# Kernel tuning notes

Hardware: AMD Instinct MI355X
Metric: run time of the kernel (lower is better)

The kernel has to match this reference:

```python
import jax, jax.numpy as jnp
import numpy as np

D_MODEL = 1024
NUM_HEADS = 16
HEAD_DIM = D_MODEL // NUM_HEADS
B, S = 2, 2048


def setup_inputs() -> dict:
    key = jax.random.key(0)
    ks = jax.random.split(key, 12)
    s = 0.02
    inp = {
        "Q": jax.random.normal(ks[0], (B, S, D_MODEL), jnp.float32),
        "K": jax.random.normal(ks[1], (B, S, D_MODEL), jnp.float32),
        "V": jax.random.normal(ks[2], (B, S, D_MODEL), jnp.float32),
        # causal mask: 1 = keep, 0 = masked (matches masked_fill(mask == 0, -inf))
        "mask": jnp.tril(jnp.ones((S, S), jnp.int32))[None, None, :, :],
        "Wq": jax.random.normal(ks[3], (D_MODEL, D_MODEL), jnp.float32) * s,
        "bq": jnp.zeros((D_MODEL,), jnp.float32),
        "Wk": jax.random.normal(ks[4], (D_MODEL, D_MODEL), jnp.float32) * s,
        "bk": jnp.zeros((D_MODEL,), jnp.float32),
        "Wv": jax.random.normal(ks[5], (D_MODEL, D_MODEL), jnp.float32) * s,
        "bv": jnp.zeros((D_MODEL,), jnp.float32),
        "Wo": jax.random.normal(ks[6], (D_MODEL, D_MODEL), jnp.float32) * s,
        "bo": jnp.zeros((D_MODEL,), jnp.float32),
    }
    return inp


def reference(Q, K, V, mask, Wq, bq, Wk, bk, Wv, bv, Wo, bo):
    b, sq, _ = Q.shape
    sk = K.shape[1]
    # linear projections (torch Linear: x @ W^T + b)
    q = Q @ Wq.T + bq
    k = K @ Wk.T + bk
    v = V @ Wv.T + bv
    # [B, H, S, Dh]
    q = q.reshape(b, sq, NUM_HEADS, HEAD_DIM).transpose(0, 2, 1, 3)
    k = k.reshape(b, sk, NUM_HEADS, HEAD_DIM).transpose(0, 2, 1, 3)
    v = v.reshape(b, sk, NUM_HEADS, HEAD_DIM).transpose(0, 2, 1, 3)
    scores = jnp.einsum("bhqd,bhkd->bhqk", q, k) / jnp.sqrt(
        jnp.asarray(HEAD_DIM, q.dtype)
    )
    scores = jnp.where(mask == 0, jnp.asarray(-jnp.inf, scores.dtype), scores)
    attn = jax.nn.softmax(scores, axis=-1)
    out = jnp.einsum("bhqk,bhkd->bhqd", attn, v)
    out = out.transpose(0, 2, 1, 3).reshape(b, sq, D_MODEL)
    return out @ Wo.T + bo
```

## Files before the change

kernel.cpp:

```cpp
#include <hip/hip_runtime.h>
#include <hip/hip_bf16.h>
#include <cstdint>
#include <cstddef>


typedef __attribute__((ext_vector_type(8))) short bf16x8;
typedef __attribute__((ext_vector_type(4))) short bf16x4;
typedef __attribute__((ext_vector_type(4))) float f32x4;
typedef __attribute__((ext_vector_type(2))) unsigned int u32x2;

constexpr int GM = 4096;
constexpr int GN = 1024;
constexpr int GK = 1024;
#define QSCALE 0.18033688011112042f

#if __has_builtin(__builtin_amdgcn_mfma_f32_16x16x16bf16_1k)
#define MFMA16(a, b, c) __builtin_amdgcn_mfma_f32_16x16x16bf16_1k((a), (b), (c), 0, 0, 0)
#elif __has_builtin(__builtin_amdgcn_mfma_f32_16x16x16_bf16)
#define MFMA16(a, b, c) __builtin_amdgcn_mfma_f32_16x16x16_bf16((a), (b), (c), 0, 0, 0)
#else
static __device__ __forceinline__ f32x4 mfma16_asm(bf16x4 a, bf16x4 b, f32x4 c) {
  asm volatile("v_mfma_f32_16x16x16_bf16 %0, %1, %2, %0" : "+v"(c) : "v"(a), "v"(b));
  return c;
}
#define MFMA16(a, b, c) mfma16_asm((a), (b), (c))
#endif

#if __has_builtin(__builtin_amdgcn_exp2f)
#define EXP2(x) __builtin_amdgcn_exp2f(x)
#else
#define EXP2(x) exp2f(x)
#endif

__device__ __forceinline__ void gload_lds16(const __hip_bfloat16* g, __hip_bfloat16* l) {
  __builtin_amdgcn_global_load_lds(
      (const __attribute__((address_space(1))) void*)g,
      (__attribute__((address_space(3))) void*)l, 16, 0, 0);
}

__device__ __forceinline__ unsigned lds_off(const void* p) {
  return (unsigned)(uintptr_t)(__attribute__((address_space(3))) const void*)p;
}

__global__ __launch_bounds__(256) void cvt7_kernel(
    const float* __restrict__ a0, const float* __restrict__ a1,
    const float* __restrict__ a2, const float* __restrict__ a3,
    const float* __restrict__ a4, const float* __restrict__ a5,
    const float* __restrict__ a6,
    __hip_bfloat16* __restrict__ o0, __hip_bfloat16* __restrict__ o1,
    __hip_bfloat16* __restrict__ o2, __hip_bfloat16* __restrict__ o3,
    __hip_bfloat16* __restrict__ o4, __hip_bfloat16* __restrict__ o5,
    __hip_bfloat16* __restrict__ o6) {
  const int z = blockIdx.z;
  const int n8 = (z < 3) ? 524288 : 131072;
  int i = blockIdx.x * 256 + threadIdx.x;
  if (i >= n8) return;
  const float* in;
  __hip_bfloat16* out;
  switch (z) {
    case 0: in = a0; out = o0; break;
    case 1: in = a1; out = o1; break;
    case 2: in = a2; out = o2; break;
    case 3: in = a3; out = o3; break;
    case 4: in = a4; out = o4; break;
    case 5: in = a5; out = o5; break;
    default: in = a6; out = o6; break;
  }
  const float4* p = (const float4*)in;
  float4 a = p[i * 2];
  float4 c = p[i * 2 + 1];
  union { __hip_bfloat16 h[8]; bf16x8 v; } u;
  u.h[0] = __float2bfloat16(a.x); u.h[1] = __float2bfloat16(a.y);
  u.h[2] = __float2bfloat16(a.z); u.h[3] = __float2bfloat16(a.w);
  u.h[4] = __float2bfloat16(c.x); u.h[5] = __float2bfloat16(c.y);
  u.h[6] = __float2bfloat16(c.z); u.h[7] = __float2bfloat16(c.w);
  *(bf16x8*)(out + (size_t)i * 8) = u.v;
}

__global__ __launch_bounds__(256) void qkv_gemm_kernel(
    const __hip_bfloat16* __restrict__ Xq, const __hip_bfloat16* __restrict__ Xk,
    const __hip_bfloat16* __restrict__ Xv,
    const __hip_bfloat16* __restrict__ Wq, const __hip_bfloat16* __restrict__ Wk,
    const __hip_bfloat16* __restrict__ Wv,
    const float* __restrict__ bq, const float* __restrict__ bk,
    const float* __restrict__ bv,
    __hip_bfloat16* __restrict__ oq, __hip_bfloat16* __restrict__ ok,
    __hip_bfloat16* __restrict__ ov) {
  __shared__ __align__(16) __hip_bfloat16 Asm[128 * 32];
  __shared__ __align__(16) __hip_bfloat16 Bsm[128 * 32];
  const int tid = threadIdx.x;
  const int l = tid & 63, w = tid >> 6;
  const int lo = l & 15, hi = l >> 4;
  const int wr = w >> 1, wc = w & 1;
  const int widx = blockIdx.x >> 3;
  const int n0 = (blockIdx.x & 7) * 128;
  const int m0 = blockIdx.y * 128;
  const int srow = (l >> 2), scol = (l & 3) * 8;

  const __hip_bfloat16* A  = (widx == 0) ? Xq : (widx == 1) ? Xk : Xv;
  const __hip_bfloat16* Bw = (widx == 0) ? Wq : (widx == 1) ? Wk : Wv;
  const float* bias        = (widx == 0) ? bq : (widx == 1) ? bk : bv;
  __hip_bfloat16* C        = (widx == 0) ? oq : (widx == 1) ? ok : ov;
  const float oscale       = (widx == 0) ? QSCALE : 1.0f;

  f32x4 acc[4][4] = {};

  for (int kt = 0; kt < GK; kt += 32) {
#pragma unroll
    for (int i = 0; i < 2; ++i) {
      const int c = i * 4 + w;
      const int row = c * 16 + srow;
      gload_lds16(A + (size_t)(m0 + row) * GK + kt + scol, &Asm[c * 512]);
      gload_lds16(Bw + (size_t)(n0 + row) * GK + kt + scol, &Bsm[c * 512]);
    }
    __syncthreads();
    bf16x8 af[4], bfr[4];
#pragma unroll
    for (int f = 0; f < 4; ++f) {
      af[f]  = *(const bf16x8*)&Asm[(wr * 64 + f * 16 + lo) * 32 + hi * 8];
      bfr[f] = *(const bf16x8*)&Bsm[(wc * 64 + f * 16 + lo) * 32 + hi * 8];
    }
#pragma unroll
    for (int i = 0; i < 4; ++i)
#pragma unroll
      for (int j = 0; j < 4; ++j)
        acc[i][j] = __builtin_amdgcn_mfma_f32_16x16x32_bf16(af[i], bfr[j], acc[i][j], 0, 0, 0);
    __syncthreads();
  }

#pragma unroll
  for (int i = 0; i < 4; ++i) {
#pragma unroll
    for (int j = 0; j < 4; ++j) {
      const int gc = n0 + wc * 64 + j * 16 + lo;
      const float bs = bias[gc];
#pragma unroll
      for (int r = 0; r < 4; ++r) {
        const int gr = m0 + wr * 64 + i * 16 + hi * 4 + r;
        C[(size_t)gr * GN + gc] = __float2bfloat16((acc[i][j][r] + bs) * oscale);
      }
    }
  }
}

__global__ __launch_bounds__(256) void gemm_out_kernel(
    const __hip_bfloat16* __restrict__ A,
    const __hip_bfloat16* __restrict__ Bw,
    const float* __restrict__ bias, float* __restrict__ C) {
  __shared__ __align__(16) __hip_bfloat16 Asm[64 * 32];
  __shared__ __align__(16) __hip_bfloat16 Bsm[128 * 32];
  const int tid = threadIdx.x;
  const int l = tid & 63, w = tid >> 6;
  const int lo = l & 15, hi = l >> 4;
  const int wr = w >> 1, wc = w & 1;
  const int m0 = blockIdx.y * 64, n0 = blockIdx.x * 128;
  const int srowA = (l >> 2), scol = (l & 3) * 8;

  f32x4 acc[2][4] = {};

  for (int kt = 0; kt < GK; kt += 32) {
    {
      const int rowA = w * 16 + srowA;
      gload_lds16(A + (size_t)(m0 + rowA) * GK + kt + scol, &Asm[w * 512]);
    }
#pragma unroll
    for (int i = 0; i < 2; ++i) {
      const int c = i * 4 + w;
      const int row = c * 16 + srowA;
      gload_lds16(Bw + (size_t)(n0 + row) * GK + kt + scol, &Bsm[c * 512]);
    }
    __syncthreads();
    bf16x8 af[2], bfr[4];
#pragma unroll
    for (int f = 0; f < 2; ++f)
      af[f] = *(const bf16x8*)&Asm[(wr * 32 + f * 16 + lo) * 32 + hi * 8];
#pragma unroll
    for (int f = 0; f < 4; ++f)
      bfr[f] = *(const bf16x8*)&Bsm[(wc * 64 + f * 16 + lo) * 32 + hi * 8];
#pragma unroll
    for (int i = 0; i < 2; ++i)
#pragma unroll
      for (int j = 0; j < 4; ++j)
        acc[i][j] = __builtin_amdgcn_mfma_f32_16x16x32_bf16(af[i], bfr[j], acc[i][j], 0, 0, 0);
    __syncthreads();
  }

#pragma unroll
  for (int i = 0; i < 2; ++i) {
#pragma unroll
    for (int j = 0; j < 4; ++j) {
      const int gc = n0 + wc * 64 + j * 16 + lo;
      const float bs = bias[gc];
#pragma unroll
      for (int r = 0; r < 4; ++r) {
        const int gr = m0 + wr * 32 + i * 16 + hi * 4 + r;
        C[(size_t)gr * GN + gc] = acc[i][j][r] + bs;
      }
    }
  }
}

__global__ __launch_bounds__(512) void attn_kernel(
    const __hip_bfloat16* __restrict__ qb,
    const __hip_bfloat16* __restrict__ kb,
    const __hip_bfloat16* __restrict__ vb,
    __hip_bfloat16* __restrict__ ob) {
  __shared__ __align__(16) __hip_bfloat16 Kl[2][64 * 64];
  __shared__ __align__(16) __hip_bfloat16 Vl[2][16 * 528];

  const int tid = threadIdx.x;
  const int l = tid & 63, w = tid >> 6;
  const int lo = l & 15, hi = l >> 4;
  const int bid = blockIdx.x;
  const int kk = bid & 15;
  const int h = (bid >> 4) & 15;
  const int b = bid >> 8;
  const int qt = b ? (15 - kk) : kk;
  const int q0 = qt * 128;

  const size_t base = (size_t)b * 2048 * 1024 + (size_t)h * 64;
  const __hip_bfloat16* qp = qb + base;
  const __hip_bfloat16* kp = kb + base;
  const __hip_bfloat16* vp = vb + base;
  __hip_bfloat16* op = ob + base;

  const int qrow = q0 + w * 16 + lo;
  bf16x8 qa[2];
  qa[0] = *(const bf16x8*)(qp + (size_t)qrow * 1024 + hi * 8);
  qa[1] = *(const bf16x8*)(qp + (size_t)qrow * 1024 + 32 + hi * 8);

  f32x4 accO[4] = {};
  float lsum = 0.f;

  const int vrow = tid >> 3;
  const int vd0 = (tid & 7) * 8;
  const int vidx = ((vrow >> 4) * 4 + (vd0 >> 4)) * 528 + (vrow & 15) * 16 + (vd0 & 15);
  const int krow = w * 8 + (l >> 3);
  const int kcolb = ((l & 7) * 16) ^ ((krow & 7) << 4);

  const unsigned vtr0 = lds_off(&Vl[0][0]) + (unsigned)l * 8;
  const unsigned vtr1 = lds_off(&Vl[1][0]) + (unsigned)l * 8;

  const int nsteps = 2 * qt + 2;

  bf16x8 vr = *(const bf16x8*)(vp + (size_t)vrow * 1024 + vd0);
  gload_lds16(kp + (size_t)krow * 1024 + (kcolb >> 1), &Kl[0][w * 512]);
  *(bf16x8*)&Vl[0][vidx] = vr;
  vr = *(const bf16x8*)(vp + (size_t)(64 + vrow) * 1024 + vd0);
  __syncthreads();

  int c = 0;

  auto step = [&](int t, int mode) {
    const int kv0 = t * 64;
    if (t + 1 < nsteps) {
      *(bf16x8*)&Vl[c ^ 1][vidx] = vr;
      gload_lds16(kp + (size_t)(kv0 + 64 + krow) * 1024 + (kcolb >> 1),
                  &Kl[c ^ 1][w * 512]);
    }
    if (t + 2 < nsteps)
      vr = *(const bf16x8*)(vp + (size_t)(kv0 + 128 + vrow) * 1024 + vd0);

    if (mode != 2) {
      const char* klbase = (const char*)&Kl[c][0];
      f32x4 sf[4];
#pragma unroll
      for (int f = 0; f < 4; ++f) {
        f32x4 s = {};
#pragma unroll
        for (int ks = 0; ks < 2; ++ks) {
          const int rl = f * 16 + lo;
          const int colb = (ks * 64 + hi * 16) ^ ((rl & 7) << 4);
          const bf16x8 kf = *(const bf16x8*)(klbase + rl * 128 + colb);
          s = __builtin_amdgcn_mfma_f32_16x16x32_bf16(kf, qa[ks], s, 0, 0, 0);
        }
        sf[f] = s;
      }

      const int qi = q0 + w * 16 + lo;
      bf16x4 pf[4];
#pragma unroll
      for (int f = 0; f < 4; ++f) {
        float p[4];
#pragma unroll
        for (int r = 0; r < 4; ++r) {
          if (mode == 1) {
            const int kvi = kv0 + f * 16 + hi * 4 + r;
            p[r] = (kvi <= qi) ? EXP2(sf[f][r]) : 0.f;
          } else {
            p[r] = EXP2(sf[f][r]);
          }
          lsum += p[r];
        }
        union { __hip_bfloat16 hh[4]; bf16x4 v; } u;
        u.hh[0] = __float2bfloat16(p[0]);
        u.hh[1] = __float2bfloat16(p[1]);
        u.hh[2] = __float2bfloat16(p[2]);
        u.hh[3] = __float2bfloat16(p[3]);
        pf[f] = u.v;
      }

      const unsigned vtr = c ? vtr1 : vtr0;
      u32x2 vv[4][4];
#pragma unroll
      for (int tc = 0; tc < 4; ++tc)
#pragma unroll
        for (int fc = 0; fc < 4; ++fc) {
          const unsigned addr = vtr + (unsigned)((tc * 4 + fc) * 1056);
          asm volatile("ds_read_b64_tr_b16 %0, %1" : "=v"(vv[tc][fc]) : "v"(addr));
        }
      asm volatile("s_waitcnt lgkmcnt(0)" ::: "memory");
      __builtin_amdgcn_sched_barrier(0);
#pragma unroll
      for (int tc = 0; tc < 4; ++tc) {
#pragma unroll
        for (int fc = 0; fc < 4; ++fc) {
          union { u32x2 u2; bf16x4 v; } cv;
          cv.u2 = vv[tc][fc];
          accO[fc] = MFMA16(pf[tc], cv.v, accO[fc]);
        }
      }
    }
    __syncthreads();
    c ^= 1;
  };

  const int nfull = 2 * qt;
  for (int t = 0; t < nfull; ++t) step(t, 0);
  step(nfull, (w < 4) ? 1 : 0);
  step(nfull + 1, (w < 4) ? 2 : 1);

  lsum += __shfl_xor(lsum, 16);
  lsum += __shfl_xor(lsum, 32);
#pragma unroll
  for (int r = 0; r < 4; ++r) {
    const float lr = __shfl(lsum, hi * 4 + r);
    const float inv = 1.f / lr;
    const int qg = q0 + w * 16 + hi * 4 + r;
#pragma unroll
    for (int fc = 0; fc < 4; ++fc)
      op[(size_t)qg * 1024 + fc * 16 + lo] = __float2bfloat16(accO[fc][r] * inv);
  }
}

extern "C" void kernel_launch(void* const* d_in, const int* in_sizes, int n_in,
                              void* d_out, int out_size, void* d_ws, size_t ws_size,
                              hipStream_t stream) {
  const float* Q  = (const float*)d_in[0];
  const float* K  = (const float*)d_in[1];
  const float* V  = (const float*)d_in[2];
  const float* Wq = (const float*)d_in[4];
  const float* bq = (const float*)d_in[5];
  const float* Wk = (const float*)d_in[6];
  const float* bk = (const float*)d_in[7];
  const float* Wv = (const float*)d_in[8];
  const float* bv = (const float*)d_in[9];
  const float* Wo = (const float*)d_in[10];
  const float* bo = (const float*)d_in[11];
  float* out = (float*)d_out;

  uint8_t* ws = (uint8_t*)d_ws;
  const size_t MB = 1024 * 1024;
  __hip_bfloat16* Qb   = (__hip_bfloat16*)(ws + 0 * MB);
  __hip_bfloat16* Kb   = (__hip_bfloat16*)(ws + 8 * MB);
  __hip_bfloat16* Vb   = (__hip_bfloat16*)(ws + 16 * MB);
  __hip_bfloat16* Wqb  = (__hip_bfloat16*)(ws + 24 * MB);
  __hip_bfloat16* Wkb  = (__hip_bfloat16*)(ws + 26 * MB);
  __hip_bfloat16* Wvb  = (__hip_bfloat16*)(ws + 28 * MB);
  __hip_bfloat16* Wob  = (__hip_bfloat16*)(ws + 30 * MB);
  __hip_bfloat16* qbuf = (__hip_bfloat16*)(ws + 32 * MB);
  __hip_bfloat16* kbuf = (__hip_bfloat16*)(ws + 40 * MB);
  __hip_bfloat16* vbuf = (__hip_bfloat16*)(ws + 48 * MB);
  __hip_bfloat16* abuf = (__hip_bfloat16*)(ws + 56 * MB);

  cvt7_kernel<<<dim3(2048, 1, 7), 256, 0, stream>>>(
      Q, K, V, Wq, Wk, Wv, Wo, Qb, Kb, Vb, Wqb, Wkb, Wvb, Wob);

  qkv_gemm_kernel<<<dim3(24, 32), 256, 0, stream>>>(
      Qb, Kb, Vb, Wqb, Wkb, Wvb, bq, bk, bv, qbuf, kbuf, vbuf);

  attn_kernel<<<2 * 16 * 16, 512, 0, stream>>>(qbuf, kbuf, vbuf, abuf);

  gemm_out_kernel<<<dim3(8, 64), 256, 0, stream>>>(abuf, Wob, bo, out);
}
```

Baseline: 225.9 us.

## Remap GEMM blocks XCD-aware, compact convert grid, raise MFMA wave priority

The conversion kernel moves from a 3D grid with many early-exiting blocks to a flat grid sized exactly to the work. Both GEMM kernels remap the flat block index so that blocks landing on the same XCD (blockIdx mod 8) cover a contiguous 2D tile region, aiming for better L2 reuse of A and B tiles. s_setprio raises wave priority around the MFMA sections in the GEMMs and the attention kernel, to favour matrix issue over other waves. The remapping changes the tile order and assumes the round-robin dispatch of blocks across XCDs.

```diff
diff --git a/kernel.cpp b/kernel.cpp
--- a/kernel.cpp
+++ b/kernel.cpp
@@ -51,10 +51,10 @@
     __hip_bfloat16* __restrict__ o2, __hip_bfloat16* __restrict__ o3,
     __hip_bfloat16* __restrict__ o4, __hip_bfloat16* __restrict__ o5,
     __hip_bfloat16* __restrict__ o6) {
-  const int z = blockIdx.z;
-  const int n8 = (z < 3) ? 524288 : 131072;
-  int i = blockIdx.x * 256 + threadIdx.x;
-  if (i >= n8) return;
+  int g = blockIdx.x;
+  int z, i;
+  if (g < 6144) { z = g >> 11; i = (g & 2047) * 256 + threadIdx.x; }
+  else { g -= 6144; z = 3 + (g >> 9); i = (g & 511) * 256 + threadIdx.x; }
   const float* in;
   __hip_bfloat16* out;
   switch (z) {
@@ -92,9 +92,15 @@
   const int l = tid & 63, w = tid >> 6;
   const int lo = l & 15, hi = l >> 4;
   const int wr = w >> 1, wc = w & 1;
-  const int widx = blockIdx.x >> 3;
-  const int n0 = (blockIdx.x & 7) * 128;
-  const int m0 = blockIdx.y * 128;
+
+  const int r = blockIdx.x & 7;
+  const int local = blockIdx.x >> 3;
+  const int rx = r & 1, ry = r >> 1;
+  const int x = rx * 12 + local % 12;
+  const int y = ry * 8 + local / 12;
+  const int widx = x >> 3;
+  const int n0 = (x & 7) * 128;
+  const int m0 = y * 128;
   const int srow = (l >> 2), scol = (l & 3) * 8;
 
   const __hip_bfloat16* A  = (widx == 0) ? Xq : (widx == 1) ? Xk : Xv;
@@ -120,11 +126,13 @@
       af[f]  = *(const bf16x8*)&Asm[(wr * 64 + f * 16 + lo) * 32 + hi * 8];
       bfr[f] = *(const bf16x8*)&Bsm[(wc * 64 + f * 16 + lo) * 32 + hi * 8];
     }
+    __builtin_amdgcn_s_setprio(1);
 #pragma unroll
     for (int i = 0; i < 4; ++i)
 #pragma unroll
       for (int j = 0; j < 4; ++j)
         acc[i][j] = __builtin_amdgcn_mfma_f32_16x16x32_bf16(af[i], bfr[j], acc[i][j], 0, 0, 0);
+    __builtin_amdgcn_s_setprio(0);
     __syncthreads();
   }
 
@@ -135,9 +143,9 @@
       const int gc = n0 + wc * 64 + j * 16 + lo;
       const float bs = bias[gc];
 #pragma unroll
-      for (int r = 0; r < 4; ++r) {
-        const int gr = m0 + wr * 64 + i * 16 + hi * 4 + r;
-        C[(size_t)gr * GN + gc] = __float2bfloat16((acc[i][j][r] + bs) * oscale);
+      for (int r2 = 0; r2 < 4; ++r2) {
+        const int gr = m0 + wr * 64 + i * 16 + hi * 4 + r2;
+        C[(size_t)gr * GN + gc] = __float2bfloat16((acc[i][j][r2] + bs) * oscale);
       }
     }
   }
@@ -153,7 +161,13 @@
   const int l = tid & 63, w = tid >> 6;
   const int lo = l & 15, hi = l >> 4;
   const int wr = w >> 1, wc = w & 1;
-  const int m0 = blockIdx.y * 64, n0 = blockIdx.x * 128;
+
+  const int r = blockIdx.x & 7;
+  const int local = blockIdx.x >> 3;
+  const int rx = r & 1, ry = r >> 1;
+  const int x = rx * 4 + (local & 3);
+  const int y = ry * 16 + (local >> 2);
+  const int m0 = y * 64, n0 = x * 128;
   const int srowA = (l >> 2), scol = (l & 3) * 8;
 
   f32x4 acc[2][4] = {};
@@ -177,11 +191,13 @@
 #pragma unroll
     for (int f = 0; f < 4; ++f)
       bfr[f] = *(const bf16x8*)&Bsm[(wc * 64 + f * 16 + lo) * 32 + hi * 8];
+    __builtin_amdgcn_s_setprio(1);
 #pragma unroll
     for (int i = 0; i < 2; ++i)
 #pragma unroll
       for (int j = 0; j < 4; ++j)
         acc[i][j] = __builtin_amdgcn_mfma_f32_16x16x32_bf16(af[i], bfr[j], acc[i][j], 0, 0, 0);
+    __builtin_amdgcn_s_setprio(0);
     __syncthreads();
   }
 
@@ -192,9 +208,9 @@
       const int gc = n0 + wc * 64 + j * 16 + lo;
       const float bs = bias[gc];
 #pragma unroll
-      for (int r = 0; r < 4; ++r) {
-        const int gr = m0 + wr * 32 + i * 16 + hi * 4 + r;
-        C[(size_t)gr * GN + gc] = acc[i][j][r] + bs;
+      for (int r2 = 0; r2 < 4; ++r2) {
+        const int gr = m0 + wr * 32 + i * 16 + hi * 4 + r2;
+        C[(size_t)gr * GN + gc] = acc[i][j][r2] + bs;
       }
     }
   }
@@ -264,6 +280,7 @@
     if (mode != 2) {
       const char* klbase = (const char*)&Kl[c][0];
       f32x4 sf[4];
+      __builtin_amdgcn_s_setprio(1);
 #pragma unroll
       for (int f = 0; f < 4; ++f) {
         f32x4 s = {};
@@ -276,6 +293,7 @@
         }
         sf[f] = s;
       }
+      __builtin_amdgcn_s_setprio(0);
 
       const int qi = q0 + w * 16 + lo;
       bf16x4 pf[4];
@@ -311,6 +329,7 @@
         }
       asm volatile("s_waitcnt lgkmcnt(0)" ::: "memory");
       __builtin_amdgcn_sched_barrier(0);
+      __builtin_amdgcn_s_setprio(1);
 #pragma unroll
       for (int tc = 0; tc < 4; ++tc) {
 #pragma unroll
@@ -320,6 +339,7 @@
           accO[fc] = MFMA16(pf[tc], cv.v, accO[fc]);
         }
       }
+      __builtin_amdgcn_s_setprio(0);
     }
     __syncthreads();
     c ^= 1;
@@ -373,13 +393,13 @@
   __hip_bfloat16* vbuf = (__hip_bfloat16*)(ws + 48 * MB);
   __hip_bfloat16* abuf = (__hip_bfloat16*)(ws + 56 * MB);
 
-  cvt7_kernel<<<dim3(2048, 1, 7), 256, 0, stream>>>(
+  cvt7_kernel<<<8192, 256, 0, stream>>>(
       Q, K, V, Wq, Wk, Wv, Wo, Qb, Kb, Vb, Wqb, Wkb, Wvb, Wob);
 
-  qkv_gemm_kernel<<<dim3(24, 32), 256, 0, stream>>>(
+  qkv_gemm_kernel<<<768, 256, 0, stream>>>(
       Qb, Kb, Vb, Wqb, Wkb, Wvb, bq, bk, bv, qbuf, kbuf, vbuf);
 
   attn_kernel<<<2 * 16 * 16, 512, 0, stream>>>(qbuf, kbuf, vbuf, abuf);
 
-  gemm_out_kernel<<<dim3(8, 64), 256, 0, stream>>>(abuf, Wob, bo, out);
-}
+  gemm_out_kernel<<<512, 256, 0, stream>>>(abuf, Wob, bo, out);
+}
```

New measurement: 221.3 us. 2.0% less time.
